# Kernel tuning notes

Hardware: AMD Instinct MI355X
Metric: run time of the kernel (lower is better)

Reference implementation:

```python
import jax, jax.numpy as jnp
import numpy as np

B, T, S, H, V = 2, 512, 400, 1024, 50257


def setup_inputs() -> dict:
    key = jax.random.key(0)
    ks = jax.random.split(key, 5)
    x = jax.random.normal(ks[0], (B, T, H), dtype=jnp.float32)
    attn_dist = jax.random.normal(ks[1], (B, T, S), dtype=jnp.float32)
    enc_batch_extend_vocab = jax.random.randint(ks[2], (B, S), 0, V)
    # learned params of nn.Linear(H, V) and nn.Linear(H, 1)
    proj_w = jax.random.normal(ks[3], (V, H), dtype=jnp.float32) * 0.02
    proj_b = jnp.zeros((V,), dtype=jnp.float32)
    pgen_w = jax.random.normal(ks[4], (1, H), dtype=jnp.float32) * 0.02
    pgen_b = jnp.zeros((1,), dtype=jnp.float32)
    return {
        "x": x,
        "attn_dist": attn_dist,
        "enc_batch_extend_vocab": enc_batch_extend_vocab,
        "temp": 1,
        "proj_w": proj_w,
        "proj_b": proj_b,
        "pgen_w": pgen_w,
        "pgen_b": pgen_b,
    }


def reference(x, attn_dist, enc_batch_extend_vocab, temp, proj_w, proj_b, pgen_w, pgen_b):
    # p_gen gate: sigmoid(Linear(H -> 1))  -> [B, T, 1]
    p_gen = jax.nn.sigmoid(jnp.einsum("bth,oh->bto", x, pgen_w) + pgen_b)
    # vocab projection: [B, T, V]
    logit = jnp.einsum("bth,vh->btv", x, proj_w) + proj_b
    vocab_dist = jax.nn.softmax(logit / temp, axis=2)
    vocab_dist_ = p_gen * vocab_dist  # [B, T, V]
    # copy distribution over source tokens: [B, T, S]
    attn = jax.nn.softmax(attn_dist / temp, axis=-1)
    attn_ = (1.0 - p_gen) * attn
    # scatter_add along vocab dim; source ids broadcast over decode steps
    idx = jnp.broadcast_to(enc_batch_extend_vocab[:, None, :], attn_.shape)  # [B, T, S]
    scat = jax.vmap(jax.vmap(lambda vd, ix, a: vd.at[ix].add(a)))
    out = scat(vocab_dist_, idx, attn_)
    return jnp.log(out + 1e-40)
```

## Files before the change

kernel.cpp:

```cpp
#include <hip/hip_runtime.h>
#include <hip/hip_bf16.h>

#define BB 2
#define TT 512
#define SS 400
#define HH 1024
#define VV 50257
#define MM (BB*TT)

#define NTILE 393
#define NT_PAD 400
#define VPAD 50304

typedef __attribute__((ext_vector_type(8))) short short8;
typedef __attribute__((ext_vector_type(4))) float f32x4;

#define AS1 __attribute__((address_space(1)))
#define AS3 __attribute__((address_space(3)))

static __device__ __forceinline__ void gl_lds16(const unsigned short* g, unsigned short* l) {
    __builtin_amdgcn_global_load_lds((const AS1 unsigned int*)(g), (AS3 unsigned int*)(l), 16, 0, 0);
}

static __device__ __forceinline__ unsigned short f2bf(float f) {
    union { float f; unsigned u; } x;
    x.f = f;
    unsigned r = x.u + 0x7FFFu + ((x.u >> 16) & 1u);
    return (unsigned short)(r >> 16);
}

static __device__ __forceinline__ float bf2f(unsigned short u) {
    union { unsigned u; float f; } x;
    x.u = ((unsigned)u) << 16;
    return x.f;
}

static __device__ __forceinline__ float get_invtemp(const int* tp) {
    int iv = *tp;
    float f;
    if (iv > 0 && iv < 100000) f = (float)iv;
    else                       f = __int_as_float(iv);
    return 1.0f / f;
}

__global__ void zero2_k(int* a, int na, int* b, int nb) {
    int i = blockIdx.x * blockDim.x + threadIdx.x;
    int st = gridDim.x * blockDim.x;
    for (int t = i; t < na; t += st) a[t] = 0;
    for (int t = i; t < nb; t += st) b[t] = 0;
}

__global__ void cvtx_pgen_k(const float* __restrict__ x, const float* __restrict__ pw,
                            const float* __restrict__ pb, unsigned short* __restrict__ xb,
                            float* __restrict__ pgen) {
    int m = blockIdx.x, tid = threadIdx.x;
    float4 v = ((const float4*)(x + (size_t)m * HH))[tid];
    ushort4 o;
    o.x = f2bf(v.x); o.y = f2bf(v.y); o.z = f2bf(v.z); o.w = f2bf(v.w);
    ((ushort4*)(xb + (size_t)m * HH))[tid] = o;
    float4 w4 = ((const float4*)pw)[tid];
    float s = v.x * w4.x + v.y * w4.y + v.z * w4.z + v.w * w4.w;
    for (int off = 32; off; off >>= 1) s += __shfl_down(s, off);
    __shared__ float red[4];
    if ((tid & 63) == 0) red[tid >> 6] = s;
    __syncthreads();
    if (tid == 0) {
        float t = red[0] + red[1] + red[2] + red[3] + pb[0];
        pgen[m] = 1.0f / (1.0f + __expf(-t));
    }
}

__global__ void cvt_w_k(const float* __restrict__ W, unsigned short* __restrict__ Wb) {
    size_t g = (size_t)blockIdx.x * 256 + threadIdx.x;
    size_t e0 = g * 8;
    int v = (int)(e0 >> 10);
    short8 o;
    if (v < VV) {
        float4 a = *(const float4*)(W + e0);
        float4 b = *(const float4*)(W + e0 + 4);
        o[0] = f2bf(a.x); o[1] = f2bf(a.y); o[2] = f2bf(a.z); o[3] = f2bf(a.w);
        o[4] = f2bf(b.x); o[5] = f2bf(b.y); o[6] = f2bf(b.z); o[7] = f2bf(b.w);
    } else {
        o = (short8){0,0,0,0,0,0,0,0};
    }
    *(short8*)(Wb + e0) = o;
}

__global__ void map_build_k(const int* __restrict__ enc, int* __restrict__ mapv) {
    int t = blockIdx.x * blockDim.x + threadIdx.x;
    if (t >= BB * SS) return;
    int b = t / SS, s = t % SS;
    int id = enc[b * SS + s];
    atomicCAS(&mapv[(size_t)b * VV + id], 0, s + 1);
}

__global__ void attn_k(const float* __restrict__ attn, const int* __restrict__ enc,
                       const int* __restrict__ mapv, const float* __restrict__ pgen,
                       float* __restrict__ Aacc, const int* __restrict__ tempp) {
    int m = blockIdx.x, tid = threadIdx.x;
    int b = m >> 9;
    float invt = get_invtemp(tempp);
    __shared__ float sv[SS];
    __shared__ float red[256];
    float loc = -1e30f;
    for (int s = tid; s < SS; s += 256) {
        float v = attn[(size_t)m * SS + s] * invt;
        sv[s] = v;
        loc = fmaxf(loc, v);
    }
    red[tid] = loc; __syncthreads();
    for (int h = 128; h; h >>= 1) { if (tid < h) red[tid] = fmaxf(red[tid], red[tid + h]); __syncthreads(); }
    float mx = red[0]; __syncthreads();
    float ls = 0.f;
    for (int s = tid; s < SS; s += 256) ls += __expf(sv[s] - mx);
    red[tid] = ls; __syncthreads();
    for (int h = 128; h; h >>= 1) { if (tid < h) red[tid] += red[tid + h]; __syncthreads(); }
    float scale = (1.0f - pgen[m]) / red[0];
    for (int s = tid; s < SS; s += 256) {
        int id = enc[b * SS + s];
        int s0 = mapv[(size_t)b * VV + id] - 1;
        atomicAdd(&Aacc[(size_t)m * SS + s0], __expf(sv[s] - mx) * scale);
    }
}

template<int LOGBF>
__global__ __launch_bounds__(256) void gemm4_k(
    const unsigned short* __restrict__ xb, const unsigned short* __restrict__ Wb,
    const float* __restrict__ bias, float* __restrict__ outf,
    unsigned short* __restrict__ outb,
    float* __restrict__ pmax, float* __restrict__ psum,
    const int* __restrict__ tempp) {
    __shared__ unsigned short As[128 * 64];
    __shared__ unsigned short Bs[128 * 64];
    __shared__ float red_mx[2][2][64];
    __shared__ float red_sm[2][2][64];

    int wgid = blockIdx.x;
    int xcd = wgid & 7;
    int l = wgid >> 3;
    int nt = xcd * 50 + (l >> 3);
    int mt = l & 7;
    if (nt >= NTILE) return;
    int m0 = mt * 128, n0 = nt * 128;

    int tid = threadIdx.x;
    int lane = tid & 63, w = tid >> 6;
    int wr = w >> 1, wc = w & 1;
    int r15 = lane & 15, kg = lane >> 4;

    size_t aoff[4], boff[4];
#pragma unroll
    for (int i = 0; i < 4; i++) {
        int q = i * 256 + tid;
        int row = q >> 3;
        int jc = (q & 7) ^ (row & 7);
        aoff[i] = (size_t)(m0 + row) * HH + jc * 8;
        boff[i] = (size_t)(n0 + row) * HH + jc * 8;
    }

    f32x4 acc[4][4];
#pragma unroll
    for (int i = 0; i < 4; i++)
#pragma unroll
        for (int j = 0; j < 4; j++) acc[i][j] = (f32x4){0.f, 0.f, 0.f, 0.f};

    for (int kt = 0; kt < HH / 64; ++kt) {
        int k0 = kt * 64;
#pragma unroll
        for (int i = 0; i < 4; i++) {
            gl_lds16(xb + aoff[i] + k0, As + (i * 256 + w * 64) * 8);
            gl_lds16(Wb + boff[i] + k0, Bs + (i * 256 + w * 64) * 8);
        }
        __syncthreads();
#pragma unroll
        for (int h = 0; h < 2; h++) {
            short8 af[4], bf[4];
#pragma unroll
            for (int mi = 0; mi < 4; mi++) {
                int row = wr * 64 + mi * 16 + r15;
                int jc = ((h << 2) | kg) ^ (row & 7);
                af[mi] = *(const short8*)&As[row * 64 + jc * 8];
            }
#pragma unroll
            for (int ni = 0; ni < 4; ni++) {
                int row = wc * 64 + ni * 16 + r15;
                int jc = ((h << 2) | kg) ^ (row & 7);
                bf[ni] = *(const short8*)&Bs[row * 64 + jc * 8];
            }
#pragma unroll
            for (int mi = 0; mi < 4; mi++)
#pragma unroll
                for (int ni = 0; ni < 4; ni++)
                    acc[mi][ni] = __builtin_amdgcn_mfma_f32_16x16x32_bf16(af[mi], bf[ni], acc[mi][ni], 0, 0, 0);
        }
        __syncthreads();
    }

    float invt = get_invtemp(tempp);
    float bv[4]; bool vld[4]; int gn[4];
#pragma unroll
    for (int ni = 0; ni < 4; ni++) {
        gn[ni] = n0 + wc * 64 + ni * 16 + r15;
        vld[ni] = gn[ni] < VV;
        bv[ni] = vld[ni] ? bias[gn[ni]] : 0.f;
    }
#pragma unroll
    for (int mi = 0; mi < 4; mi++) {
#pragma unroll
        for (int j = 0; j < 4; j++) {
            float mx = -1e30f;
#pragma unroll
            for (int ni = 0; ni < 4; ni++)
                if (vld[ni]) mx = fmaxf(mx, (acc[mi][ni][j] + bv[ni]) * invt);
            float sm = 0.f;
#pragma unroll
            for (int ni = 0; ni < 4; ni++)
                if (vld[ni]) sm += __expf((acc[mi][ni][j] + bv[ni]) * invt - mx);
#pragma unroll
            for (int o = 1; o < 16; o <<= 1) {
                float m2 = __shfl_xor(mx, o);
                float s2 = __shfl_xor(sm, o);
                float nm = fmaxf(mx, m2);
                sm = sm * __expf(mx - nm) + s2 * __expf(m2 - nm);
                mx = nm;
            }
            if (r15 == 0) {
                red_mx[wr][wc][mi * 16 + kg * 4 + j] = mx;
                red_sm[wr][wc][mi * 16 + kg * 4 + j] = sm;
            }
        }
    }
#pragma unroll
    for (int ni = 0; ni < 4; ni++) {
        if (vld[ni]) {
#pragma unroll
            for (int mi = 0; mi < 4; mi++) {
                int gmb = m0 + wr * 64 + mi * 16 + (kg << 2);
#pragma unroll
                for (int j = 0; j < 4; j++) {
                    if (LOGBF)
                        outb[(size_t)(gmb + j) * VPAD + gn[ni]] = f2bf(acc[mi][ni][j] + bv[ni]);
                    else
                        outf[(size_t)(gmb + j) * VV + gn[ni]] = acc[mi][ni][j] + bv[ni];
                }
            }
        }
    }
    __syncthreads();
    if (tid < 128) {
        int r = tid & 63, wr2 = tid >> 6;
        float m1 = red_mx[wr2][0][r], s1 = red_sm[wr2][0][r];
        float m2 = red_mx[wr2][1][r], s2 = red_sm[wr2][1][r];
        float nm = fmaxf(m1, m2);
        float s = s1 * __expf(m1 - nm) + s2 * __expf(m2 - nm);
        int gm = m0 + wr2 * 64 + r;
        pmax[(size_t)gm * NT_PAD + nt] = nm;
        psum[(size_t)gm * NT_PAD + nt] = s;
    }
}

__global__ void lse_wave_k(const float* __restrict__ pmax, const float* __restrict__ psum,
                           float* __restrict__ lse) {
    int gw = (blockIdx.x * blockDim.x + threadIdx.x) >> 6;
    int ln = threadIdx.x & 63;
    if (gw >= MM) return;
    const float* pm = pmax + (size_t)gw * NT_PAD;
    const float* ps = psum + (size_t)gw * NT_PAD;
    float M = -1e30f, S = 0.f;
    for (int t = ln; t < NTILE; t += 64) {
        float m2 = pm[t], s2 = ps[t];
        float nm = fmaxf(M, m2);
        S = S * __expf(M - nm) + s2 * __expf(m2 - nm);
        M = nm;
    }
#pragma unroll
    for (int o = 1; o < 64; o <<= 1) {
        float m2 = __shfl_xor(M, o);
        float s2 = __shfl_xor(S, o);
        float nm = fmaxf(M, m2);
        S = S * __expf(M - nm) + s2 * __expf(m2 - nm);
        M = nm;
    }
    if (ln == 0) lse[gw] = M + __logf(S);
}

__global__ void finalize_bf_k(const unsigned short* __restrict__ logb,
                              float* __restrict__ out, const float* __restrict__ pgen,
                              const float* __restrict__ lse, const int* __restrict__ mapv,
                              const float* __restrict__ Aacc, const int* __restrict__ tempp) {
    int m = blockIdx.y;
    int c = blockIdx.x * 256 + threadIdx.x;
    int v0 = c * 4;
    if (v0 >= VV) return;
    int b = m >> 9;
    float invt = get_invtemp(tempp);
    float pg = pgen[m], L = lse[m];
    ushort4 lb = *(const ushort4*)(logb + (size_t)m * VPAD + v0);
    const int* mrow = mapv + (size_t)b * VV;
    const float* arow = Aacc + (size_t)m * SS;
    size_t base = (size_t)m * VV;
    unsigned short ls[4] = {lb.x, lb.y, lb.z, lb.w};
#pragma unroll
    for (int j = 0; j < 4; j++) {
        int v = v0 + j;
        if (v < VV) {
            float p = pg * __expf(bf2f(ls[j]) * invt - L);
            int jm = mrow[v];
            if (jm) p += arow[jm - 1];
            out[base + v] = __logf(p + 1e-40f);
        }
    }
}

__global__ void finalize_k(float* __restrict__ out, const float* __restrict__ pgen,
                           const float* __restrict__ lse, const int* __restrict__ mapv,
                           const float* __restrict__ Aacc, const int* __restrict__ tempp) {
    int m = blockIdx.y;
    int b = m >> 9;
    float invt = get_invtemp(tempp);
    float pg = pgen[m], L = lse[m];
    size_t base = (size_t)m * VV;
    const int* mrow = mapv + (size_t)b * VV;
    const float* arow = Aacc + (size_t)m * SS;
    int sk = (-m) & 3;
    int nchunk = (VV - sk) >> 2;
    int c = blockIdx.x * 256 + threadIdx.x;
    if (c < nchunk) {
        int v0 = sk + 4 * c;
        float4 l4 = *(const float4*)(out + base + v0);
        float xs[4] = {l4.x, l4.y, l4.z, l4.w};
        float rs[4];
#pragma unroll
        for (int j = 0; j < 4; j++) {
            float p = pg * __expf(xs[j] * invt - L);
            int jm = mrow[v0 + j];
            if (jm) p += arow[jm - 1];
            rs[j] = __logf(p + 1e-40f);
        }
        float4 o4 = {rs[0], rs[1], rs[2], rs[3]};
        *(float4*)(out + base + v0) = o4;
    }
    if (blockIdx.x == 0 && threadIdx.x == 0) {
        for (int v = 0; v < sk; v++) {
            float p = pg * __expf(out[base + v] * invt - L);
            int jm = mrow[v];
            if (jm) p += arow[jm - 1];
            out[base + v] = __logf(p + 1e-40f);
        }
        for (int v = sk + 4 * nchunk; v < VV; v++) {
            float p = pg * __expf(out[base + v] * invt - L);
            int jm = mrow[v];
            if (jm) p += arow[jm - 1];
            out[base + v] = __logf(p + 1e-40f);
        }
    }
}

__global__ __launch_bounds__(256) void gemm_old_k(
    const unsigned short* __restrict__ xb, const float* __restrict__ W,
    const float* __restrict__ bias, float* __restrict__ out) {
    __shared__ unsigned short As[128][40];
    __shared__ unsigned short Bs[128][40];
    int bid = blockIdx.x;
    int mt = bid & 7;
    int nt = bid >> 3;
    int m0 = mt * 128, n0 = nt * 128;
    int tid = threadIdx.x;
    int lid = tid & 63, w = tid >> 6;
    int wr = w >> 1, wc = w & 1;
    int row16 = lid & 15, kg = lid >> 4;

    f32x4 acc[4][4];
#pragma unroll
    for (int i = 0; i < 4; i++)
#pragma unroll
        for (int j = 0; j < 4; j++) acc[i][j] = (f32x4){0.f, 0.f, 0.f, 0.f};

    int tr = tid >> 3;
    int tc = (tid & 7) << 2;

    for (int kt = 0; kt < HH / 32; ++kt) {
        int k0 = kt * 32;
        __syncthreads();
#pragma unroll
        for (int i = 0; i < 4; i++) {
            int r = tr + 32 * i;
            ushort4 a4 = *(const ushort4*)&xb[(size_t)(m0 + r) * HH + k0 + tc];
            *(ushort4*)&As[r][tc] = a4;
            int v = n0 + r; v = (v < VV) ? v : (VV - 1);
            float4 w4 = *(const float4*)&W[(size_t)v * HH + k0 + tc];
            ushort4 b4;
            b4.x = f2bf(w4.x); b4.y = f2bf(w4.y); b4.z = f2bf(w4.z); b4.w = f2bf(w4.w);
            *(ushort4*)&Bs[r][tc] = b4;
        }
        __syncthreads();
        short8 af[4], bf[4];
#pragma unroll
        for (int i = 0; i < 4; i++) {
            af[i] = *(const short8*)&As[wr * 64 + i * 16 + row16][kg * 8];
            bf[i] = *(const short8*)&Bs[wc * 64 + i * 16 + row16][kg * 8];
        }
#pragma unroll
        for (int mi = 0; mi < 4; mi++)
#pragma unroll
            for (int ni = 0; ni < 4; ni++)
                acc[mi][ni] = __builtin_amdgcn_mfma_f32_16x16x32_bf16(af[mi], bf[ni], acc[mi][ni], 0, 0, 0);
    }
#pragma unroll
    for (int ni = 0; ni < 4; ni++) {
        int gnv = n0 + wc * 64 + ni * 16 + row16;
        if (gnv < VV) {
            float bvv = bias[gnv];
#pragma unroll
            for (int mi = 0; mi < 4; mi++) {
                int gmb = m0 + wr * 64 + mi * 16 + (kg << 2);
#pragma unroll
                for (int j = 0; j < 4; j++)
                    out[(size_t)(gmb + j) * VV + gnv] = acc[mi][ni][j] + bvv;
            }
        }
    }
}

__global__ void rowreduce_k(const float* __restrict__ out, float* __restrict__ lse,
                            const int* __restrict__ tempp) {
    int m = blockIdx.x, tid = threadIdx.x;
    float invt = get_invtemp(tempp);
    const float* row = out + (size_t)m * VV;
    int sk = (-m) & 3;
    int nchunk = (VV - sk) >> 2;
    float mi = -1e30f, si = 0.f;
    for (int c = tid; c < nchunk; c += 256) {
        float4 x4 = *(const float4*)(row + sk + 4 * c);
        float xs[4] = {x4.x, x4.y, x4.z, x4.w};
#pragma unroll
        for (int j = 0; j < 4; j++) {
            float x = xs[j] * invt;
            float nm = fmaxf(mi, x);
            si = si * __expf(mi - nm) + __expf(x - nm);
            mi = nm;
        }
    }
    if (tid == 0) {
        for (int v = 0; v < sk; v++) {
            float x = row[v] * invt;
            float nm = fmaxf(mi, x);
            si = si * __expf(mi - nm) + __expf(x - nm);
            mi = nm;
        }
        for (int v = sk + 4 * nchunk; v < VV; v++) {
            float x = row[v] * invt;
            float nm = fmaxf(mi, x);
            si = si * __expf(mi - nm) + __expf(x - nm);
            mi = nm;
        }
    }
    __shared__ float sm[256], ss[256];
    sm[tid] = mi; ss[tid] = si; __syncthreads();
    for (int h = 128; h; h >>= 1) {
        if (tid < h) {
            float m2 = sm[tid + h], s2 = ss[tid + h];
            float nm = fmaxf(sm[tid], m2);
            ss[tid] = ss[tid] * __expf(sm[tid] - nm) + s2 * __expf(m2 - nm);
            sm[tid] = nm;
        }
        __syncthreads();
    }
    if (tid == 0) lse[m] = sm[0] + __logf(ss[0]);
}

extern "C" void kernel_launch(void* const* d_in, const int* in_sizes, int n_in,
                              void* d_out, int out_size, void* d_ws, size_t ws_size,
                              hipStream_t stream) {
    const float* x      = (const float*)d_in[0];
    const float* attn   = (const float*)d_in[1];
    const int*   enc    = (const int*)d_in[2];
    const int*   temp   = (const int*)d_in[3];
    const float* proj_w = (const float*)d_in[4];
    const float* proj_b = (const float*)d_in[5];
    const float* pgen_w = (const float*)d_in[6];
    const float* pgen_b = (const float*)d_in[7];
    float* out = (float*)d_out;

    char* ws = (char*)d_ws;
    const size_t WB_BYTES = (size_t)VPAD * HH * 2;

    size_t o_wb   = 0;
    size_t o_xb   = o_wb + WB_BYTES;
    size_t o_pgen = o_xb + 2097152;
    size_t o_lse  = o_pgen + 4096;
    size_t o_map  = o_lse + 4096;
    size_t o_aacc = o_map + 402432;
    size_t o_pmax = o_aacc + (size_t)MM * SS * 4;
    size_t o_psum = o_pmax + (size_t)MM * NT_PAD * 4;
    size_t o_logb = o_psum + (size_t)MM * NT_PAD * 4;
    size_t need_mid = o_logb;
    size_t need_big = o_logb + (size_t)MM * VPAD * 2;

    if (ws_size >= need_mid) {
        unsigned short* wb   = (unsigned short*)(ws + o_wb);
        unsigned short* xb   = (unsigned short*)(ws + o_xb);
        float*          pgen = (float*)(ws + o_pgen);
        float*          lse  = (float*)(ws + o_lse);
        int*            mapv = (int*)(ws + o_map);
        float*          Aacc = (float*)(ws + o_aacc);
        float*          pmax = (float*)(ws + o_pmax);
        float*          psum = (float*)(ws + o_psum);
        unsigned short* logb = (unsigned short*)(ws + o_logb);

        zero2_k<<<512, 256, 0, stream>>>(mapv, BB * VV, (int*)Aacc, MM * SS);
        cvtx_pgen_k<<<MM, 256, 0, stream>>>(x, pgen_w, pgen_b, xb, pgen);
        cvt_w_k<<<(VPAD * HH / 8 + 255) / 256, 256, 0, stream>>>(proj_w, wb);
        map_build_k<<<4, 256, 0, stream>>>(enc, mapv);
        attn_k<<<MM, 256, 0, stream>>>(attn, enc, mapv, pgen, Aacc, temp);
        if (ws_size >= need_big) {
            gemm4_k<1><<<8 * NT_PAD, 256, 0, stream>>>(xb, wb, proj_b, out, logb, pmax, psum, temp);
            lse_wave_k<<<256, 256, 0, stream>>>(pmax, psum, lse);
            finalize_bf_k<<<dim3((VV + 1023) / 1024, MM), 256, 0, stream>>>(logb, out, pgen, lse, mapv, Aacc, temp);
        } else {
            gemm4_k<0><<<8 * NT_PAD, 256, 0, stream>>>(xb, wb, proj_b, out, logb, pmax, psum, temp);
            lse_wave_k<<<256, 256, 0, stream>>>(pmax, psum, lse);
            finalize_k<<<dim3(50, MM), 256, 0, stream>>>(out, pgen, lse, mapv, Aacc, temp);
        }
    } else {
        unsigned short* xb   = (unsigned short*)(ws + 0);
        float*          pgen = (float*)(ws + 2097152);
        float*          lse  = (float*)(ws + 2101248);
        int*            mapv = (int*)(ws + 2105344);
        float*          Aacc = (float*)(ws + 2507776);

        zero2_k<<<512, 256, 0, stream>>>(mapv, BB * VV, (int*)Aacc, MM * SS);
        cvtx_pgen_k<<<MM, 256, 0, stream>>>(x, pgen_w, pgen_b, xb, pgen);
        map_build_k<<<4, 256, 0, stream>>>(enc, mapv);
        attn_k<<<MM, 256, 0, stream>>>(attn, enc, mapv, pgen, Aacc, temp);
        gemm_old_k<<<8 * NTILE, 256, 0, stream>>>(xb, proj_w, proj_b, out);
        rowreduce_k<<<MM, 256, 0, stream>>>(out, lse, temp);
        finalize_k<<<dim3(50, MM), 256, 0, stream>>>(out, pgen, lse, mapv, Aacc, temp);
    }
}
```

Measured before the change: 435.3 us.

## Load MFMA operands directly from global memory with register double buffering

The bf16 GEMM no longer stages A and B tiles through LDS with global_load_lds and barriers. Each lane now loads its MFMA fragments straight from global memory into registers, using two alternating register sets so the next k-step's loads overlap the current MFMAs. This removes LDS traffic and the per-iteration __syncthreads. In exchange, each fragment is fetched from global/L2 by both waves that share it, with no cross-wave reuse, and register pressure rises from the fully unrolled 32-step loop.

```diff
diff --git a/kernel.cpp b/kernel.cpp
--- a/kernel.cpp
+++ b/kernel.cpp
@@ -14,13 +14,6 @@
 
 typedef __attribute__((ext_vector_type(8))) short short8;
 typedef __attribute__((ext_vector_type(4))) float f32x4;
-
-#define AS1 __attribute__((address_space(1)))
-#define AS3 __attribute__((address_space(3)))
-
-static __device__ __forceinline__ void gl_lds16(const unsigned short* g, unsigned short* l) {
-    __builtin_amdgcn_global_load_lds((const AS1 unsigned int*)(g), (AS3 unsigned int*)(l), 16, 0, 0);
-}
 
 static __device__ __forceinline__ unsigned short f2bf(float f) {
     union { float f; unsigned u; } x;
@@ -124,14 +117,12 @@
 }
 
 template<int LOGBF>
-__global__ __launch_bounds__(256) void gemm4_k(
+__global__ __launch_bounds__(256) void gemm7_k(
     const unsigned short* __restrict__ xb, const unsigned short* __restrict__ Wb,
     const float* __restrict__ bias, float* __restrict__ outf,
     unsigned short* __restrict__ outb,
     float* __restrict__ pmax, float* __restrict__ psum,
     const int* __restrict__ tempp) {
-    __shared__ unsigned short As[128 * 64];
-    __shared__ unsigned short Bs[128 * 64];
     __shared__ float red_mx[2][2][64];
     __shared__ float red_sm[2][2][64];
 
@@ -148,14 +139,12 @@
     int wr = w >> 1, wc = w & 1;
     int r15 = lane & 15, kg = lane >> 4;
 
-    size_t aoff[4], boff[4];
+    const unsigned short* pa[4];
+    const unsigned short* pb[4];
 #pragma unroll
     for (int i = 0; i < 4; i++) {
-        int q = i * 256 + tid;
-        int row = q >> 3;
-        int jc = (q & 7) ^ (row & 7);
-        aoff[i] = (size_t)(m0 + row) * HH + jc * 8;
-        boff[i] = (size_t)(n0 + row) * HH + jc * 8;
+        pa[i] = xb + (size_t)(m0 + wr * 64 + i * 16 + r15) * HH + kg * 8;
+        pb[i] = Wb + (size_t)(n0 + wc * 64 + i * 16 + r15) * HH + kg * 8;
     }
 
     f32x4 acc[4][4];
@@ -164,37 +153,31 @@
 #pragma unroll
         for (int j = 0; j < 4; j++) acc[i][j] = (f32x4){0.f, 0.f, 0.f, 0.f};
 
-    for (int kt = 0; kt < HH / 64; ++kt) {
-        int k0 = kt * 64;
-#pragma unroll
-        for (int i = 0; i < 4; i++) {
-            gl_lds16(xb + aoff[i] + k0, As + (i * 256 + w * 64) * 8);
-            gl_lds16(Wb + boff[i] + k0, Bs + (i * 256 + w * 64) * 8);
-        }
-        __syncthreads();
-#pragma unroll
-        for (int h = 0; h < 2; h++) {
-            short8 af[4], bf[4];
-#pragma unroll
-            for (int mi = 0; mi < 4; mi++) {
-                int row = wr * 64 + mi * 16 + r15;
-                int jc = ((h << 2) | kg) ^ (row & 7);
-                af[mi] = *(const short8*)&As[row * 64 + jc * 8];
-            }
-#pragma unroll
-            for (int ni = 0; ni < 4; ni++) {
-                int row = wc * 64 + ni * 16 + r15;
-                int jc = ((h << 2) | kg) ^ (row & 7);
-                bf[ni] = *(const short8*)&Bs[row * 64 + jc * 8];
-            }
-#pragma unroll
-            for (int mi = 0; mi < 4; mi++)
-#pragma unroll
-                for (int ni = 0; ni < 4; ni++)
-                    acc[mi][ni] = __builtin_amdgcn_mfma_f32_16x16x32_bf16(af[mi], bf[ni], acc[mi][ni], 0, 0, 0);
-        }
-        __syncthreads();
-    }
+    short8 a0[4], b0[4], a1[4], b1[4];
+
+#define LOADF(A, B, step) do { \
+    _Pragma("unroll") for (int i = 0; i < 4; i++) A[i] = *(const short8*)(pa[i] + (step) * 32); \
+    _Pragma("unroll") for (int i = 0; i < 4; i++) B[i] = *(const short8*)(pb[i] + (step) * 32); \
+} while (0)
+#define MFMA16(A, B) do { \
+    _Pragma("unroll") for (int mi = 0; mi < 4; mi++) \
+    _Pragma("unroll") for (int ni = 0; ni < 4; ni++) \
+        acc[mi][ni] = __builtin_amdgcn_mfma_f32_16x16x32_bf16(A[mi], B[ni], acc[mi][ni], 0, 0, 0); \
+} while (0)
+
+    LOADF(a0, b0, 0);
+#pragma unroll
+    for (int kk = 0; kk < 15; ++kk) {
+        LOADF(a1, b1, 2 * kk + 1);
+        MFMA16(a0, b0);
+        LOADF(a0, b0, 2 * kk + 2);
+        MFMA16(a1, b1);
+    }
+    LOADF(a1, b1, 31);
+    MFMA16(a0, b0);
+    MFMA16(a1, b1);
+#undef LOADF
+#undef MFMA16
 
     float invt = get_invtemp(tempp);
     float bv[4]; bool vld[4]; int gn[4];
@@ -514,11 +497,11 @@
         map_build_k<<<4, 256, 0, stream>>>(enc, mapv);
         attn_k<<<MM, 256, 0, stream>>>(attn, enc, mapv, pgen, Aacc, temp);
         if (ws_size >= need_big) {
-            gemm4_k<1><<<8 * NT_PAD, 256, 0, stream>>>(xb, wb, proj_b, out, logb, pmax, psum, temp);
+            gemm7_k<1><<<8 * NT_PAD, 256, 0, stream>>>(xb, wb, proj_b, out, logb, pmax, psum, temp);
             lse_wave_k<<<256, 256, 0, stream>>>(pmax, psum, lse);
             finalize_bf_k<<<dim3((VV + 1023) / 1024, MM), 256, 0, stream>>>(logb, out, pgen, lse, mapv, Aacc, temp);
         } else {
-            gemm4_k<0><<<8 * NT_PAD, 256, 0, stream>>>(xb, wb, proj_b, out, logb, pmax, psum, temp);
+            gemm7_k<0><<<8 * NT_PAD, 256, 0, stream>>>(xb, wb, proj_b, out, logb, pmax, psum, temp);
             lse_wave_k<<<256, 256, 0, stream>>>(pmax, psum, lse);
             finalize_k<<<dim3(50, MM), 256, 0, stream>>>(out, pgen, lse, mapv, Aacc, temp);
         }
```

Result: slower. 671.6 us (+54.3%).
